# Performance work log

Hardware: AMD Instinct MI355X
Metric: run time of the kernel (lower is better)

The kernel has to match this reference:

```python
import jax, jax.numpy as jnp
import numpy as np

B, T, C, H = 4, 1024, 512, 8
HD = C // H
N_NODE, F_DIM, TOTAL_DIM = 64, 8, 16
SCALE = 1.0 / np.sqrt(HD)


def _build_mask():
    # causal tril with every (total_dim-1 mod total_dim)-th COLUMN zeroed
    m = np.tril(np.ones((T, T), dtype=np.float32))
    m[:, TOTAL_DIM - 1::TOTAL_DIM] = 0.0
    return jnp.asarray(m)

MASK = _build_mask()  # (T, T), 1 = keep, 0 = mask


def setup_inputs() -> dict:
    key = jax.random.key(0)
    ks = jax.random.split(key, 12)
    s = 0.02
    return {
        "x": jax.random.normal(ks[0], (B, T, C), dtype=jnp.float32),
        "attn_bias": jax.random.normal(ks[1], (H, N_NODE, N_NODE), dtype=jnp.float32) * 0.1,
        "Wq": jax.random.normal(ks[2], (C, C), dtype=jnp.float32) * s,
        "bq": jax.random.normal(ks[3], (C,), dtype=jnp.float32) * s,
        "Wk": jax.random.normal(ks[4], (C, C), dtype=jnp.float32) * s,
        "bk": jax.random.normal(ks[5], (C,), dtype=jnp.float32) * s,
        "Wv": jax.random.normal(ks[6], (C, C), dtype=jnp.float32) * s,
        "bv": jax.random.normal(ks[7], (C,), dtype=jnp.float32) * s,
        "Wp": jax.random.normal(ks[8], (C, C), dtype=jnp.float32) * s,
        "bp": jax.random.normal(ks[9], (C,), dtype=jnp.float32) * s,
    }


def reference(x, attn_bias, Wq, bq, Wk, bk, Wv, bv, Wp, bp):
    Bx, Tx, Cx = x.shape

    def heads(W, b):  # (B,T,C) -> (B,H,T,HD); torch Linear is x @ W.T + b
        return (x @ W.T + b).reshape(Bx, Tx, H, HD).transpose(0, 2, 1, 3)

    q, k, v = heads(Wq, bq), heads(Wk, bk), heads(Wv, bv)

    # repeat_interleave + repeat expansion == kron(attn_bias, ones(f_dim, f_dim))
    d = N_NODE * F_DIM
    bias = jnp.repeat(jnp.repeat(attn_bias, F_DIM, axis=1), F_DIM, axis=2)  # (H, d, d)
    padded_bias = jnp.zeros((H, Tx, Tx), dtype=x.dtype).at[:, :d, :d].set(bias)

    att = jnp.einsum('bhqd,bhkd->bhqk', q, k) * SCALE + padded_bias[None]
    neg = jnp.asarray(-jnp.inf, dtype=att.dtype)
    att = jnp.where(MASK[None, None, :Tx, :Tx] == 0, neg, att)
    att = jax.nn.softmax(att, axis=-1)

    y = jnp.einsum('bhqk,bhkd->bhqd', att, v)
    y = y.transpose(0, 2, 1, 3).reshape(Bx, Tx, Cx)
    return y @ Wp.T + bp
```

## Files before the change

kernel.cpp:

```cpp
#include <hip/hip_runtime.h>

#define T_SEQ 1024
#define C_DIM 512
#define H_HEADS 8
#define HDIM 64
#define B_BATCH 4
#define M_ROWS (B_BATCH * T_SEQ)
#define NSPLIT_TOT 40

typedef __attribute__((ext_vector_type(8))) short short8;
typedef __attribute__((ext_vector_type(4))) float f32x4;

__device__ __forceinline__ unsigned short f2bf(float f) {
    unsigned u = __builtin_bit_cast(unsigned, f);
    u += 0x7FFFu + ((u >> 16) & 1u);
    return (unsigned short)(u >> 16);
}

__device__ __constant__ unsigned char BX_OF[NSPLIT_TOT] =
    {0,1,2,3,4,4,5,5,6,6,7,7,8,8,8,9,9,9,10,10,10,11,11,11,
     12,12,12,12,13,13,13,13,14,14,14,14,15,15,15,15};
__device__ __constant__ unsigned char SP_OF[NSPLIT_TOT] =
    {0,0,0,0,0,1,0,1,0,1,0,1,0,1,2,0,1,2,0,1,2,0,1,2,
     0,1,2,3,0,1,2,3,0,1,2,3,0,1,2,3};
__device__ __constant__ unsigned char CUM_OF[16] =
    {0,1,2,3,4,6,8,10,12,15,18,21,24,28,32,36};

__global__ __launch_bounds__(256) void cast_all(
    const float* __restrict__ x,
    const float* __restrict__ wq, const float* __restrict__ wk,
    const float* __restrict__ wv, const float* __restrict__ wp,
    unsigned short* __restrict__ xb,
    unsigned short* __restrict__ wqb, unsigned short* __restrict__ wkb,
    unsigned short* __restrict__ wvb, unsigned short* __restrict__ wpb)
{
    const long NX = (long)M_ROWS * C_DIM;
    const long NW = (long)C_DIM * C_DIM;
    long i4 = (long)blockIdx.x * blockDim.x + threadIdx.x;
    long base = i4 * 4;
    const float* src; unsigned short* dst; long off;
    if (base < NX) { src = x; dst = xb; off = base; }
    else {
        long r = base - NX;
        int w = (int)(r >> 18);
        off = r & (NW - 1);
        switch (w) {
            case 0:  src = wq; dst = wqb; break;
            case 1:  src = wk; dst = wkb; break;
            case 2:  src = wv; dst = wvb; break;
            default: src = wp; dst = wpb; break;
        }
    }
    float4 v = *(const float4*)(src + off);
    ushort4 o;
    o.x = f2bf(v.x); o.y = f2bf(v.y); o.z = f2bf(v.z); o.w = f2bf(v.w);
    *(ushort4*)(dst + off) = o;
}

__device__ __forceinline__ void gemm_body(
    const unsigned short* __restrict__ A,
    const unsigned short* __restrict__ W,
    const float* __restrict__ bias,
    unsigned short* __restrict__ Obf,
    float* __restrict__ Of,
    int mode)
{
    __shared__ __align__(16) unsigned short Al[64 * 72];
    __shared__ __align__(16) unsigned short Bl[64 * 72];

    const int tid  = threadIdx.x;
    const int w    = tid >> 6;
    const int lane = tid & 63;
    const int quad = lane >> 4;
    const int l16  = lane & 15;
    const int m0   = blockIdx.x * 64;
    const int n0   = blockIdx.y * 64;

    f32x4 acc[4] = {};

    for (int k0 = 0; k0 < 512; k0 += 64) {
        __syncthreads();
        for (int it = 0; it < 2; ++it) {
            int ch = tid + 256 * it;
            int r = ch >> 3, c8 = ch & 7;
            *(short8*)&Al[r * 72 + c8 * 8] =
                *(const short8*)&A[(long)(m0 + r) * 512 + k0 + c8 * 8];
            *(short8*)&Bl[r * 72 + c8 * 8] =
                *(const short8*)&W[(long)(n0 + r) * 512 + k0 + c8 * 8];
        }
        __syncthreads();
        for (int s = 0; s < 2; ++s) {
            short8 af = *(const short8*)&Al[(16 * w + l16) * 72 + 32 * s + 8 * quad];
            for (int ct = 0; ct < 4; ++ct) {
                short8 bf = *(const short8*)&Bl[(16 * ct + l16) * 72 + 32 * s + 8 * quad];
                acc[ct] = __builtin_amdgcn_mfma_f32_16x16x32_bf16(af, bf, acc[ct], 0, 0, 0);
            }
        }
    }

    for (int ct = 0; ct < 4; ++ct) {
        int col = n0 + 16 * ct + l16;
        float bv = bias[col];
        for (int reg = 0; reg < 4; ++reg) {
            int row = m0 + 16 * w + 4 * quad + reg;
            float v = acc[ct][reg] + bv;
            if (mode == 2) {
                Of[(long)row * 512 + col] = v;
            } else {
                int b = row >> 10, t = row & 1023;
                int h = col >> 6,  hd = col & 63;
                long idx = (mode == 0)
                    ? ((((long)(b * H_HEADS + h)) * T_SEQ + t) * HDIM + hd)
                    : ((((long)(b * H_HEADS + h)) * HDIM + hd) * T_SEQ + t);
                Obf[idx] = f2bf(v);
            }
        }
    }
}

__global__ __launch_bounds__(256) void gemm_qkv(
    const unsigned short* __restrict__ A,
    const unsigned short* __restrict__ Wq, const unsigned short* __restrict__ Wk,
    const unsigned short* __restrict__ Wv,
    const float* __restrict__ bq, const float* __restrict__ bk, const float* __restrict__ bv,
    unsigned short* __restrict__ Q, unsigned short* __restrict__ K,
    unsigned short* __restrict__ V)
{
    const unsigned short* W; const float* b; unsigned short* O; int mode;
    if (blockIdx.z == 0)      { W = Wq; b = bq; O = Q; mode = 0; }
    else if (blockIdx.z == 1) { W = Wk; b = bk; O = K; mode = 0; }
    else                      { W = Wv; b = bv; O = V; mode = 1; }
    gemm_body(A, W, b, O, nullptr, mode);
}

__global__ __launch_bounds__(256) void gemm_out_k(
    const unsigned short* __restrict__ A, const unsigned short* __restrict__ W,
    const float* __restrict__ bias, float* __restrict__ O)
{
    gemm_body(A, W, bias, nullptr, O, 2);
}

__global__ __launch_bounds__(256) void attn_split(
    const unsigned short* __restrict__ Q, const unsigned short* __restrict__ K,
    const unsigned short* __restrict__ Vt, const float* __restrict__ attn_bias,
    float* __restrict__ Opart, float* __restrict__ mpart, float* __restrict__ lpart)
{
    __shared__ __align__(16) unsigned short Kl[64 * 72];
    __shared__ __align__(16) unsigned short Vl[64 * 72];
    __shared__ __align__(16) unsigned short Pl[4][16 * 72];
    __shared__ float biasl[8][64];

    const int tid  = threadIdx.x;
    const int w    = tid >> 6;
    const int lane = tid & 63;
    const int quad = lane >> 4;
    const int l16  = lane & 15;
    const int sidx = blockIdx.x;
    const int bh   = blockIdx.y;
    const int h    = bh & 7;
    const int bx   = BX_OF[sidx];
    const int sp   = SP_OF[sidx];
    const int q0   = bx * 64;
    const int kt0  = sp * 4;
    const int kt1  = min(kt0 + 4, bx + 1);

    if (q0 < 512 && sp < 2) {
        for (int i = tid; i < 512; i += 256) {
            int nq = (q0 >> 3) + (i >> 6);
            biasl[i >> 6][i & 63] = attn_bias[h * 4096 + nq * 64 + (i & 63)];
        }
    }

    const unsigned short* Qbh = Q  + (long)bh * T_SEQ * HDIM;
    const unsigned short* Kbh = K  + (long)bh * T_SEQ * HDIM;
    const unsigned short* Vbh = Vt + (long)bh * HDIM * T_SEQ;

    short8 qf[2];
    {
        int qr = q0 + 16 * w + l16;
        qf[0] = *(const short8*)&Qbh[(long)qr * HDIM + 8 * quad];
        qf[1] = *(const short8*)&Qbh[(long)qr * HDIM + 32 + 8 * quad];
    }

    f32x4 oacc[4] = {};
    float mrow[4] = {-INFINITY, -INFINITY, -INFINITY, -INFINITY};
    float lrow[4] = {0.f, 0.f, 0.f, 0.f};

    for (int kt = kt0; kt < kt1; ++kt) {
        const int k0 = kt * 64;
        __syncthreads();
        for (int it = 0; it < 2; ++it) {
            int ch = tid + 256 * it;
            int r = ch >> 3, c8 = ch & 7;
            *(short8*)&Kl[r * 72 + c8 * 8] =
                *(const short8*)&Kbh[(long)(k0 + r) * HDIM + c8 * 8];
            *(short8*)&Vl[r * 72 + c8 * 8] =
                *(const short8*)&Vbh[(long)r * T_SEQ + k0 + c8 * 8];
        }
        __syncthreads();

        f32x4 s[4] = {};
        for (int st = 0; st < 2; ++st) {
            for (int ct = 0; ct < 4; ++ct) {
                short8 bf = *(const short8*)&Kl[(16 * ct + l16) * 72 + 32 * st + 8 * quad];
                s[ct] = __builtin_amdgcn_mfma_f32_16x16x32_bf16(qf[st], bf, s[ct], 0, 0, 0);
            }
        }

        const int qrb = q0 + 16 * w + 4 * quad;
        float rmax[4] = {-INFINITY, -INFINITY, -INFINITY, -INFINITY};
        for (int ct = 0; ct < 4; ++ct) {
            int kcol = k0 + 16 * ct + l16;
            for (int reg = 0; reg < 4; ++reg) {
                int qrow = qrb + reg;
                float v = s[ct][reg] * 0.125f;
                if (qrow < 512 && kcol < 512)
                    v += biasl[(qrow >> 3) & 7][kcol >> 3];
                bool keep = (kcol <= qrow) && ((kcol & 15) != 15);
                v = keep ? v : -INFINITY;
                s[ct][reg] = v;
                rmax[reg] = fmaxf(rmax[reg], v);
            }
        }
        for (int off = 1; off < 16; off <<= 1)
            for (int reg = 0; reg < 4; ++reg)
                rmax[reg] = fmaxf(rmax[reg], __shfl_xor(rmax[reg], off));

        float alpha[4];
        for (int reg = 0; reg < 4; ++reg) {
            float mnew = fmaxf(mrow[reg], rmax[reg]);
            alpha[reg] = __expf(mrow[reg] - mnew);
            mrow[reg] = mnew;
        }

        float rsum[4] = {0.f, 0.f, 0.f, 0.f};
        for (int ct = 0; ct < 4; ++ct) {
            for (int reg = 0; reg < 4; ++reg) {
                float p = __expf(s[ct][reg] - mrow[reg]);
                rsum[reg] += p;
                Pl[w][(4 * quad + reg) * 72 + 16 * ct + l16] = f2bf(p);
            }
        }
        for (int off = 1; off < 16; off <<= 1)
            for (int reg = 0; reg < 4; ++reg)
                rsum[reg] += __shfl_xor(rsum[reg], off);
        for (int reg = 0; reg < 4; ++reg)
            lrow[reg] = lrow[reg] * alpha[reg] + rsum[reg];
        for (int ct = 0; ct < 4; ++ct)
            for (int reg = 0; reg < 4; ++reg)
                oacc[ct][reg] *= alpha[reg];

        for (int st = 0; st < 2; ++st) {
            short8 af = *(const short8*)&Pl[w][l16 * 72 + 32 * st + 8 * quad];
            for (int ct = 0; ct < 4; ++ct) {
                short8 bf = *(const short8*)&Vl[(16 * ct + l16) * 72 + 32 * st + 8 * quad];
                oacc[ct] = __builtin_amdgcn_mfma_f32_16x16x32_bf16(af, bf, oacc[ct], 0, 0, 0);
            }
        }
    }

    const long p = (long)bh * NSPLIT_TOT + sidx;
    float* Op = Opart + p * 4096;
    for (int ct = 0; ct < 4; ++ct)
        for (int reg = 0; reg < 4; ++reg)
            Op[(16 * w + 4 * quad + reg) * 64 + 16 * ct + l16] = oacc[ct][reg];
    if (l16 == 0) {
        for (int reg = 0; reg < 4; ++reg) {
            int qr = 16 * w + 4 * quad + reg;
            mpart[p * 64 + qr] = mrow[reg];
            lpart[p * 64 + qr] = lrow[reg];
        }
    }
}

__global__ __launch_bounds__(256) void attn_combine(
    const float* __restrict__ Opart, const float* __restrict__ mpart,
    const float* __restrict__ lpart, unsigned short* __restrict__ Y)
{
    const int bx = blockIdx.x, bh = blockIdx.y;
    const int b = bh >> 3, h = bh & 7;
    const int ns = (bx >> 2) + 1;
    const long p0 = (long)bh * NSPLIT_TOT + CUM_OF[bx];
    const int tid = threadIdx.x;
    const int qr = tid >> 2;
    const int hs = (tid & 3) * 16;

    float m[4], l[4];
    for (int s = 0; s < ns; ++s) {
        m[s] = mpart[(p0 + s) * 64 + qr];
        l[s] = lpart[(p0 + s) * 64 + qr];
    }
    float ms = -INFINITY;
    for (int s = 0; s < ns; ++s) ms = fmaxf(ms, m[s]);
    float L = 0.f, sc[4];
    for (int s = 0; s < ns; ++s) { sc[s] = __expf(m[s] - ms); L += l[s] * sc[s]; }

    float acc[16] = {};
    for (int s = 0; s < ns; ++s) {
        const float4* op = (const float4*)(Opart + (p0 + s) * 4096 + qr * 64 + hs);
        float f = sc[s];
        for (int j4 = 0; j4 < 4; ++j4) {
            float4 v = op[j4];
            acc[4 * j4 + 0] += f * v.x; acc[4 * j4 + 1] += f * v.y;
            acc[4 * j4 + 2] += f * v.z; acc[4 * j4 + 3] += f * v.w;
        }
    }
    float inv = 1.f / L;
    int q = bx * 64 + qr;
    unsigned short* y = Y + ((long)b * T_SEQ + q) * C_DIM + h * HDIM + hs;
    for (int j4 = 0; j4 < 4; ++j4) {
        ushort4 o;
        o.x = f2bf(acc[4 * j4 + 0] * inv); o.y = f2bf(acc[4 * j4 + 1] * inv);
        o.z = f2bf(acc[4 * j4 + 2] * inv); o.w = f2bf(acc[4 * j4 + 3] * inv);
        *(ushort4*)(y + 4 * j4) = o;
    }
}

extern "C" void kernel_launch(void* const* d_in, const int* in_sizes, int n_in,
                              void* d_out, int out_size, void* d_ws, size_t ws_size,
                              hipStream_t stream)
{
    const float* x         = (const float*)d_in[0];
    const float* attn_bias = (const float*)d_in[1];
    const float* Wq = (const float*)d_in[2]; const float* bq = (const float*)d_in[3];
    const float* Wk = (const float*)d_in[4]; const float* bk = (const float*)d_in[5];
    const float* Wv = (const float*)d_in[6]; const float* bv = (const float*)d_in[7];
    const float* Wp = (const float*)d_in[8]; const float* bp = (const float*)d_in[9];
    float* out = (float*)d_out;

    const long NX = (long)M_ROWS * C_DIM;
    const long NW = (long)C_DIM * C_DIM;

    unsigned short* xb  = (unsigned short*)d_ws;
    unsigned short* wqb = xb  + NX;
    unsigned short* wkb = wqb + NW;
    unsigned short* wvb = wkb + NW;
    unsigned short* wpb = wvb + NW;
    unsigned short* Qb  = wpb + NW;
    unsigned short* Kb  = Qb  + NX;
    unsigned short* Vtb = Kb  + NX;
    unsigned short* Yb  = Vtb + NX;
    float* Opart = (float*)(Yb + NX);
    float* mpart = Opart + (long)32 * NSPLIT_TOT * 4096;
    float* lpart = mpart + (long)32 * NSPLIT_TOT * 64;

    long n4 = (NX + 4 * NW) / 4;
    cast_all<<<dim3((unsigned)(n4 / 256)), 256, 0, stream>>>(
        x, Wq, Wk, Wv, Wp, xb, wqb, wkb, wvb, wpb);

    gemm_qkv<<<dim3(M_ROWS / 64, C_DIM / 64, 3), 256, 0, stream>>>(
        xb, wqb, wkb, wvb, bq, bk, bv, Qb, Kb, Vtb);

    attn_split<<<dim3(NSPLIT_TOT, B_BATCH * H_HEADS), 256, 0, stream>>>(
        Qb, Kb, Vtb, attn_bias, Opart, mpart, lpart);

    attn_combine<<<dim3(T_SEQ / 64, B_BATCH * H_HEADS), 256, 0, stream>>>(
        Opart, mpart, lpart, Yb);

    gemm_out_k<<<dim3(M_ROWS / 64, C_DIM / 64), 256, 0, stream>>>(
        Yb, wpb, bp, out);
}
```

Before: 142.6 us.

## Use 128x128 GEMM tiles with direct global-to-LDS loads and XOR swizzle

The shared GEMM body moves from 64x64 to 128x128 output tiles, with each wave computing a 64x64 sub-block as a 4x4 grid of MFMAs. Operand tiles are loaded straight into LDS with global_load_lds, and an XOR swizzle replaces the padded layout to avoid bank conflicts. The V projection swaps MFMA operands so the transposed stores run along t and coalesce. Larger tiles cut redundant global loads and raise MFMA density, but the grids for the QKV and output GEMMs shrink, which reduces how much of the GPU the launches can fill.

```diff
diff --git a/kernel.cpp b/kernel.cpp
--- a/kernel.cpp
+++ b/kernel.cpp
@@ -15,6 +15,12 @@
     unsigned u = __builtin_bit_cast(unsigned, f);
     u += 0x7FFFu + ((u >> 16) & 1u);
     return (unsigned short)(u >> 16);
+}
+
+__device__ __forceinline__ void gload_lds16(const unsigned short* g, unsigned short* l) {
+    __builtin_amdgcn_global_load_lds(
+        (const __attribute__((address_space(1))) unsigned int*)(const void*)g,
+        (__attribute__((address_space(3))) unsigned int*)(void*)l, 16, 0, 0);
 }
 
 __device__ __constant__ unsigned char BX_OF[NSPLIT_TOT] =
@@ -65,54 +71,80 @@
     float* __restrict__ Of,
     int mode)
 {
-    __shared__ __align__(16) unsigned short Al[64 * 72];
-    __shared__ __align__(16) unsigned short Bl[64 * 72];
+    __shared__ __align__(16) unsigned short Atile[128 * 64];
+    __shared__ __align__(16) unsigned short Btile[128 * 64];
 
     const int tid  = threadIdx.x;
     const int w    = tid >> 6;
     const int lane = tid & 63;
     const int quad = lane >> 4;
     const int l16  = lane & 15;
-    const int m0   = blockIdx.x * 64;
-    const int n0   = blockIdx.y * 64;
-
-    f32x4 acc[4] = {};
+    const int m0   = blockIdx.x * 128;
+    const int n0   = blockIdx.y * 128;
+    const int wr   = 64 * (w >> 1);
+    const int wc   = 64 * (w & 1);
+
+    f32x4 acc[4][4] = {};
+
+    const int lr = lane >> 3;
+    const int lc = lane & 7;
 
     for (int k0 = 0; k0 < 512; k0 += 64) {
         __syncthreads();
-        for (int it = 0; it < 2; ++it) {
-            int ch = tid + 256 * it;
-            int r = ch >> 3, c8 = ch & 7;
-            *(short8*)&Al[r * 72 + c8 * 8] =
-                *(const short8*)&A[(long)(m0 + r) * 512 + k0 + c8 * 8];
-            *(short8*)&Bl[r * 72 + c8 * 8] =
-                *(const short8*)&W[(long)(n0 + r) * 512 + k0 + c8 * 8];
+        for (int i = 0; i < 4; ++i) {
+            int r0 = 32 * w + 8 * i;
+            int r  = r0 + lr;
+            int c  = lc ^ (r & 7);
+            gload_lds16(&A[(long)(m0 + r) * 512 + k0 + c * 8], &Atile[r0 * 64]);
+            gload_lds16(&W[(long)(n0 + r) * 512 + k0 + c * 8], &Btile[r0 * 64]);
         }
         __syncthreads();
-        for (int s = 0; s < 2; ++s) {
-            short8 af = *(const short8*)&Al[(16 * w + l16) * 72 + 32 * s + 8 * quad];
-            for (int ct = 0; ct < 4; ++ct) {
-                short8 bf = *(const short8*)&Bl[(16 * ct + l16) * 72 + 32 * s + 8 * quad];
-                acc[ct] = __builtin_amdgcn_mfma_f32_16x16x32_bf16(af, bf, acc[ct], 0, 0, 0);
-            }
-        }
-    }
-
-    for (int ct = 0; ct < 4; ++ct) {
-        int col = n0 + 16 * ct + l16;
-        float bv = bias[col];
-        for (int reg = 0; reg < 4; ++reg) {
-            int row = m0 + 16 * w + 4 * quad + reg;
-            float v = acc[ct][reg] + bv;
-            if (mode == 2) {
-                Of[(long)row * 512 + col] = v;
-            } else {
-                int b = row >> 10, t = row & 1023;
-                int h = col >> 6,  hd = col & 63;
-                long idx = (mode == 0)
-                    ? ((((long)(b * H_HEADS + h)) * T_SEQ + t) * HDIM + hd)
-                    : ((((long)(b * H_HEADS + h)) * HDIM + hd) * T_SEQ + t);
-                Obf[idx] = f2bf(v);
+
+        for (int st = 0; st < 2; ++st) {
+            const int pc = ((4 * st + quad) ^ (l16 & 7)) * 8;
+            short8 af[4], bf[4];
+            for (int i = 0; i < 4; ++i)
+                af[i] = *(const short8*)&Atile[(wr + 16 * i + l16) * 64 + pc];
+            for (int j = 0; j < 4; ++j)
+                bf[j] = *(const short8*)&Btile[(wc + 16 * j + l16) * 64 + pc];
+            for (int i = 0; i < 4; ++i)
+                for (int j = 0; j < 4; ++j)
+                    acc[i][j] = (mode == 1)
+                        ? __builtin_amdgcn_mfma_f32_16x16x32_bf16(bf[j], af[i], acc[i][j], 0, 0, 0)
+                        : __builtin_amdgcn_mfma_f32_16x16x32_bf16(af[i], bf[j], acc[i][j], 0, 0, 0);
+        }
+    }
+
+    if (mode == 1) {
+        for (int j = 0; j < 4; ++j) {
+            for (int reg = 0; reg < 4; ++reg) {
+                int n = n0 + wc + 16 * j + 4 * quad + reg;
+                int h = n >> 6, hd = n & 63;
+                float bv = bias[n];
+                for (int i = 0; i < 4; ++i) {
+                    int t = m0 + wr + 16 * i + l16;
+                    int b = t >> 10, tl = t & 1023;
+                    Obf[(((long)(b * H_HEADS + h)) * HDIM + hd) * T_SEQ + tl] =
+                        f2bf(acc[i][j][reg] + bv);
+                }
+            }
+        }
+    } else {
+        for (int j = 0; j < 4; ++j) {
+            int col = n0 + wc + 16 * j + l16;
+            float bv = bias[col];
+            for (int i = 0; i < 4; ++i) {
+                for (int reg = 0; reg < 4; ++reg) {
+                    int row = m0 + wr + 16 * i + 4 * quad + reg;
+                    float v = acc[i][j][reg] + bv;
+                    if (mode == 2) {
+                        Of[(long)row * 512 + col] = v;
+                    } else {
+                        int b = row >> 10, t = row & 1023;
+                        int h = col >> 6,  hd = col & 63;
+                        Obf[(((long)(b * H_HEADS + h)) * T_SEQ + t) * HDIM + hd] = f2bf(v);
+                    }
+                }
             }
         }
     }
@@ -348,7 +380,7 @@
     cast_all<<<dim3((unsigned)(n4 / 256)), 256, 0, stream>>>(
         x, Wq, Wk, Wv, Wp, xb, wqb, wkb, wvb, wpb);
 
-    gemm_qkv<<<dim3(M_ROWS / 64, C_DIM / 64, 3), 256, 0, stream>>>(
+    gemm_qkv<<<dim3(M_ROWS / 128, C_DIM / 128, 3), 256, 0, stream>>>(
         xb, wqb, wkb, wvb, bq, bk, bv, Qb, Kb, Vtb);
 
     attn_split<<<dim3(NSPLIT_TOT, B_BATCH * H_HEADS), 256, 0, stream>>>(
@@ -357,6 +389,6 @@
     attn_combine<<<dim3(T_SEQ / 64, B_BATCH * H_HEADS), 256, 0, stream>>>(
         Opart, mpart, lpart, Yb);
 
-    gemm_out_k<<<dim3(M_ROWS / 64, C_DIM / 64), 256, 0, stream>>>(
+    gemm_out_k<<<dim3(M_ROWS / 128, C_DIM / 128), 256, 0, stream>>>(
         Yb, wpb, bp, out);
 }
```

New measurement: 145.0 us. About the same (+1.7%).
